# Kernel optimization log

Measured on AMD Instinct MI355X. Metric: run time of the kernel, lower is better.

The kernel has to match this reference:

```python
import jax, jax.numpy as jnp
import numpy as np


def conv2d(x, w, b, pad=0, groups=1):
    y = jax.lax.conv_general_dilated(
        x, w, (1, 1), [(pad, pad), (pad, pad)],
        dimension_numbers=('NCHW', 'OIHW', 'NCHW'), feature_group_count=groups)
    return y + b[None, :, None, None]


def layernorm(x, w, b, eps=1e-5):
    # per-pixel LayerNorm over channel dim (matches to_3d -> nn.LayerNorm(dim) -> to_4d)
    mu = x.mean(1, keepdims=True)
    var = ((x - mu) ** 2).mean(1, keepdims=True)
    return (x - mu) * jax.lax.rsqrt(var + eps) * w[None, :, None, None] + b[None, :, None, None]


def setup_inputs():
    key = jax.random.key(0)
    ks = jax.random.split(key, 16)
    B, C, H, W = 1, 64, 64, 64
    heads, dh = 8, 8
    inner = heads * dh          # 64
    hid_lc = 32                 # max(16, inner // 2)
    hid_f = 4 * C               # 256, ffn_expansion_factor = 4
    def s(k, shape, fan):
        return (jax.random.normal(k, shape, jnp.float32) / np.float32(np.sqrt(fan)))
    return {
        'x': jax.random.normal(ks[0], (B, C, H, W), jnp.float32),
        'luma': jax.random.uniform(ks[1], (B, 1, H, W), jnp.float32),
        'ln1_w': jnp.ones((C,), jnp.float32), 'ln1_b': jnp.zeros((C,), jnp.float32),
        'qkv_w': s(ks[2], (3 * inner, C, 1, 1), C), 'qkv_b': jnp.zeros((3 * inner,), jnp.float32),
        'proj_w': s(ks[3], (C, inner, 1, 1), inner), 'proj_b': jnp.zeros((C,), jnp.float32),
        'lc1_w': s(ks[4], (hid_lc, 1, 3, 3), 9), 'lc1_b': jnp.zeros((hid_lc,), jnp.float32),
        'lc2_w': s(ks[5], (hid_lc, hid_lc, 3, 3), 9 * hid_lc), 'lc2_b': jnp.zeros((hid_lc,), jnp.float32),
        'gam_w': s(ks[6], (inner, hid_lc, 1, 1), hid_lc), 'gam_b': jnp.zeros((inner,), jnp.float32),
        'bet_w': s(ks[7], (inner, hid_lc, 1, 1), hid_lc), 'bet_b': jnp.zeros((inner,), jnp.float32),
        'alpha': jnp.float32(0.1),
        'ln2_w': jnp.ones((C,), jnp.float32), 'ln2_b': jnp.zeros((C,), jnp.float32),
        'ffn1_w': s(ks[8], (hid_f, C, 1, 1), C), 'ffn1_b': jnp.zeros((hid_f,), jnp.float32),
        'dw_w': s(ks[9], (hid_f, 1, 3, 3), 9), 'dw_b': jnp.zeros((hid_f,), jnp.float32),
        'ffn2_w': s(ks[10], (C, hid_f, 1, 1), hid_f), 'ffn2_b': jnp.zeros((C,), jnp.float32),
    }


def reference(x, luma, ln1_w, ln1_b, qkv_w, qkv_b, proj_w, proj_b,
              lc1_w, lc1_b, lc2_w, lc2_b, gam_w, gam_b, bet_w, bet_b, alpha,
              ln2_w, ln2_b, ffn1_w, ffn1_b, dw_w, dw_b, ffn2_w, ffn2_b):
    B, C, H, W = x.shape
    heads = 8
    N = H * W
    # --- attention branch ---
    xn = layernorm(x, ln1_w, ln1_b)
    qkv = conv2d(xn, qkv_w, qkv_b)             # [B, 3*inner, H, W]
    inner = qkv.shape[1] // 3
    dh = inner // heads

    def to_bhnd(t):  # b (h d) x y -> b h (x y) d
        return t.reshape(B, heads, dh, N).transpose(0, 1, 3, 2)

    q, k, v = [to_bhnd(t) for t in jnp.split(qkv, 3, axis=1)]
    # luma conditioning
    h1 = jax.nn.relu(conv2d(luma, lc1_w, lc1_b, pad=1))
    h1 = jax.nn.relu(conv2d(h1, lc2_w, lc2_b, pad=1))
    g = to_bhnd(conv2d(h1, gam_w, gam_b))
    bt = to_bhnd(conv2d(h1, bet_w, bet_b))
    q = g * q + bt
    k = g * k + bt
    v = g * v + bt
    # additive luma bias on q (avg_pool2d 3x3, count_include_pad=True -> fixed /9)
    invL = 1.0 - luma
    invL = jax.lax.reduce_window(invL, 0.0, jax.lax.add, (1, 1, 3, 3), (1, 1, 1, 1),
                                 [(0, 0), (0, 0), (1, 1), (1, 1)]) / 9.0
    invL = invL.reshape(B, N)
    invL = invL - invL.mean(-1, keepdims=True)
    q = q + alpha * invL[:, None, :, None]
    scale = dh ** -0.5
    attn = jax.nn.softmax(jnp.einsum('bhid,bhjd->bhij', q, k) * scale, axis=-1)
    out = jnp.einsum('bhij,bhjd->bhid', attn, v)
    out = out.transpose(0, 1, 3, 2).reshape(B, inner, H, W)
    x = x + conv2d(out, proj_w, proj_b)
    # --- ConvFFN branch ---
    y = layernorm(x, ln2_w, ln2_b)
    y = conv2d(y, ffn1_w, ffn1_b)
    y = conv2d(y, dw_w, dw_b, pad=1, groups=y.shape[1])
    y = jax.nn.gelu(y, approximate=False)
    y = conv2d(y, ffn2_w, ffn2_b)
    return x + y
```

## Files before the change

### kernel.cpp

```cpp
#include <hip/hip_runtime.h>
#include <math.h>

#define NPIX 4096
#define IMG 64
#define NBLK 512

typedef __attribute__((ext_vector_type(8))) short bf16x8;
typedef __attribute__((ext_vector_type(4))) float floatx4;
typedef __attribute__((ext_vector_type(4))) unsigned int uintx4;

__device__ __forceinline__ unsigned int split_pack(float x) {
  unsigned int u = __float_as_uint(x);
  unsigned int hif = u & 0xffff0000u;
  float lof = x - __uint_as_float(hif);
  return (u >> 16) | (__float_as_uint(lof) & 0xffff0000u);
}

__device__ __forceinline__ unsigned int pack_hi2(float a, float b) {
  return __builtin_amdgcn_perm(__float_as_uint(b), __float_as_uint(a),
                               0x07060302u);
}

__device__ __forceinline__ void stA_f32(float* p, float v) {
  __hip_atomic_store(p, v, __ATOMIC_RELAXED, __HIP_MEMORY_SCOPE_AGENT);
}
__device__ __forceinline__ void stA_u32(void* p, unsigned int v) {
  __hip_atomic_store((unsigned int*)p, v, __ATOMIC_RELAXED,
                     __HIP_MEMORY_SCOPE_AGENT);
}
__device__ __forceinline__ void stA_u64(void* p, unsigned long long v) {
  __hip_atomic_store((unsigned long long*)p, v, __ATOMIC_RELAXED,
                     __HIP_MEMORY_SCOPE_AGENT);
}
__device__ __forceinline__ unsigned int ldA(const unsigned int* p) {
  return __hip_atomic_load(p, __ATOMIC_RELAXED, __HIP_MEMORY_SCOPE_AGENT);
}
__device__ __forceinline__ unsigned int addA(unsigned int* p) {
  return __hip_atomic_fetch_add(p, 1u, __ATOMIC_RELAXED,
                                __HIP_MEMORY_SCOPE_AGENT);
}

__device__ __forceinline__ void gbar(unsigned int* base, int bid) {
  __syncthreads();
  if (threadIdx.x == 0) {
    int g = bid >> 6;
    unsigned int* ga = base + g * 32;
    unsigned int old = addA(ga);
    if (old == 63u) {
      addA(base + 256);
      while (ldA(base + 256) < 8u) __builtin_amdgcn_s_sleep(1);
      stA_u32(ga + 16, 1u);
    } else {
      while (ldA(ga + 16) == 0u) __builtin_amdgcn_s_sleep(2);
    }
    asm volatile("" ::: "memory");
  }
  __syncthreads();
}

struct S1 {
  float lum[144];
  float sw1[288];
  float tin[32][100];
  float swt[4][32][9];
  float red[64];
};
struct S2 {
  float xs[64][32];
  float wsh[64][64];
  float h2s[32][32];
  float wgs[32][64];
  float wbs[32][64];
  float pss[8][32];
  float pqq[8][32];
  float mu[32];
  float rs[32];
};
struct S4 {
  float at[64][34];
  float wsh[64][64];
  float xsl[64][34];
  float ps[16][32];
  float pq[16][32];
  float mus[32];
  float rss[32];
};
struct S5 {
  float xs2[16][260];
  float wshT[32][260];
};
union SU {
  S1 s1;
  S2 s2;
  S4 s4;
  S5 s5;
};

__global__ void init_kernel(unsigned int* __restrict__ ctr,
                            unsigned short* __restrict__ cbuf) {
  int t = threadIdx.x;
#pragma unroll
  for (int i = 0; i < 8; i++) ctr[t + i * 256] = 0u;
  if (t < 16) cbuf[t] = (t < 8) ? 0x3F80 : 0;
}

__global__ __launch_bounds__(256, 3) void fused_kernel(
    const float* __restrict__ x, const float* __restrict__ luma,
    const float* __restrict__ lc1w, const float* __restrict__ lc1b,
    const float* __restrict__ lc2w, const float* __restrict__ lc2b,
    const float* __restrict__ ln1w, const float* __restrict__ ln1b,
    const float* __restrict__ qkvW, const float* __restrict__ qkvB,
    const float* __restrict__ gamW, const float* __restrict__ gamB,
    const float* __restrict__ betW, const float* __restrict__ betB,
    const float* __restrict__ alpha, const float* __restrict__ projW,
    const float* __restrict__ projB, const float* __restrict__ ln2w,
    const float* __restrict__ ln2b, const float* __restrict__ ffn1W,
    const float* __restrict__ ffn1B, const float* __restrict__ dww,
    const float* __restrict__ dwb, const float* __restrict__ ffn2W,
    const float* __restrict__ ffn2B, float* __restrict__ out,
    float* __restrict__ pooled, float* __restrict__ bsums,
    unsigned short* __restrict__ cbuf, unsigned short* __restrict__ qhl,
    unsigned short* __restrict__ khl, unsigned short* __restrict__ vthx,
    unsigned short* __restrict__ vtlx, float* __restrict__ pacc,
    float* __restrict__ pl, float* __restrict__ x1, float* __restrict__ f1,
    float* __restrict__ h2, unsigned int* __restrict__ ctr) {
  __shared__ SU u;
  int bid = blockIdx.x;
  int tid = threadIdx.x;

  {
    int tile = bid >> 3, ocg = bid & 7;
    int ty0 = (tile >> 3) * 8, tx0 = (tile & 7) * 8;
    float(&lum)[144] = u.s1.lum;
    float(&sw1)[288] = u.s1.sw1;
    float(&tin)[32][100] = u.s1.tin;
    float(&swt)[4][32][9] = u.s1.swt;
    float(&red)[64] = u.s1.red;
    if (tid < 144) {
      int py = tid / 12, px = tid - py * 12;
      int gy = ty0 + py - 2, gx = tx0 + px - 2;
      lum[tid] = (gy >= 0 && gy < IMG && gx >= 0 && gx < IMG)
                     ? luma[gy * IMG + gx]
                     : 0.f;
    }
    for (int idx = tid; idx < 288; idx += 256) sw1[idx] = lc1w[idx];
    for (int idx = tid; idx < 1152; idx += 256) {
      int o = idx / 288, r = idx - o * 288;
      swt[o][r / 9][r % 9] = lc2w[(ocg * 4 + o) * 288 + r];
    }
    __syncthreads();
    for (int idx = tid; idx < 3200; idx += 256) {
      int ic = idx / 100, pos = idx - ic * 100;
      int py = pos / 10, px = pos - py * 10;
      int gy = ty0 + py - 1, gx = tx0 + px - 1;
      float v = 0.f;
      if (gy >= 0 && gy < IMG && gx >= 0 && gx < IMG) {
        float s = lc1b[ic];
        const float* wp = &sw1[ic * 9];
#pragma unroll
        for (int dy = 0; dy < 3; dy++)
#pragma unroll
          for (int dx = 0; dx < 3; dx++)
            s = fmaf(wp[dy * 3 + dx], lum[(py + dy) * 12 + px + dx], s);
        v = fmaxf(s, 0.f);
      }
      tin[ic][pos] = v;
    }
    __syncthreads();
    int o = tid >> 6, pix = tid & 63;
    int ly = pix >> 3, lx = pix & 7;
    int p = (ty0 + ly) * IMG + tx0 + lx;
    float acc = lc2b[ocg * 4 + o];
    for (int ic = 0; ic < 32; ic++) {
      float v[9];
#pragma unroll
      for (int dy = 0; dy < 3; dy++)
#pragma unroll
        for (int dx = 0; dx < 3; dx++)
          v[dy * 3 + dx] = tin[ic][(ly + dy) * 10 + lx + dx];
#pragma unroll
      for (int t = 0; t < 9; t++) acc = fmaf(swt[o][ic][t], v[t], acc);
    }
    stA_f32(&h2[(ocg * 4 + o) * NPIX + p], fmaxf(acc, 0.f));
    if (ocg == 0) {
      if (tid < 64) {
        int gy = ty0 + ly, gx = tx0 + lx;
        float sv = 0.f;
#pragma unroll
        for (int dy = 0; dy < 3; dy++)
#pragma unroll
          for (int dx = 0; dx < 3; dx++)
            sv += lum[(ly + dy + 1) * 12 + lx + dx + 1];
        float cy = 3.f - (gy == 0 ? 1.f : 0.f) - (gy == 63 ? 1.f : 0.f);
        float cx = 3.f - (gx == 0 ? 1.f : 0.f) - (gx == 63 ? 1.f : 0.f);
        float pv = (cy * cx - sv) * (1.f / 9.f);
        stA_f32(&pooled[p], pv);
        red[tid] = pv;
      }
      __syncthreads();
      for (int st = 32; st > 0; st >>= 1) {
        if (tid < st) red[tid] += red[tid + st];
        __syncthreads();
      }
      if (tid == 0) stA_f32(&bsums[tile], red[0]);
    }
  }
  gbar(ctr + 0, bid);

  {
    const float QSCALE = 0.35355339059327376f * 1.4426950408889634f;
    float(&xs)[64][32] = u.s2.xs;
    float(&wsh)[64][64] = u.s2.wsh;
    float(&h2s)[32][32] = u.s2.h2s;
    float(&wgs)[32][64] = u.s2.wgs;
    float(&wbs)[32][64] = u.s2.wbs;
    float(&pss)[8][32] = u.s2.pss;
    float(&pqq)[8][32] = u.s2.pqq;
    float(&mu)[32] = u.s2.mu;
    float(&rs)[32] = u.s2.rs;
    int n0 = (bid & 127) * 32, part = bid >> 7;
    int m0 = (part < 2 ? part : 2) * 64;
    {
      int e = tid * 2;
      int c = e >> 3, off = (e & 7) * 4;
      *(float4*)&xs[c][off] = *(const float4*)&x[c * NPIX + n0 + off];
      int e1 = e + 1;
      int c1 = e1 >> 3, off1 = (e1 & 7) * 4;
      *(float4*)&xs[c1][off1] = *(const float4*)&x[c1 * NPIX + n0 + off1];
    }
    {
      int m = tid >> 2, kg = (tid & 3) * 16;
      const float4* wr = (const float4*)&qkvW[(m0 + m) * 64 + kg];
      float4 w0 = wr[0], w1 = wr[1], w2 = wr[2], w3 = wr[3];
      float wv[16] = {w0.x, w0.y, w0.z, w0.w, w1.x, w1.y, w1.z, w1.w,
                      w2.x, w2.y, w2.z, w2.w, w3.x, w3.y, w3.z, w3.w};
#pragma unroll
      for (int j = 0; j < 16; j++) wsh[kg + j][m] = wv[j];
    }
    {
      int k = tid >> 3, nf = (tid & 7) * 4;
      *(float4*)&h2s[k][nf] = *(const float4*)&h2[k * NPIX + n0 + nf];
    }
    {
      int m = tid >> 2, kg = (tid & 3) * 8;
      const float4* g0 = (const float4*)&gamW[m * 32 + kg];
      float4 a = g0[0], b4 = g0[1];
      float gv[8] = {a.x, a.y, a.z, a.w, b4.x, b4.y, b4.z, b4.w};
#pragma unroll
      for (int j = 0; j < 8; j++) wgs[kg + j][m] = gv[j];
      const float4* bb0 = (const float4*)&betW[m * 32 + kg];
      float4 c4 = bb0[0], d4 = bb0[1];
      float bv[8] = {c4.x, c4.y, c4.z, c4.w, d4.x, d4.y, d4.z, d4.w};
#pragma unroll
      for (int j = 0; j < 8; j++) wbs[kg + j][m] = bv[j];
    }
    __syncthreads();
    {
      int p = tid & 31, i = tid >> 5;
      float s = 0.f, q = 0.f;
#pragma unroll
      for (int j = 0; j < 8; j++) {
        float xv = xs[i * 8 + j][p];
        s += xv;
        q = fmaf(xv, xv, q);
      }
      pss[i][p] = s;
      pqq[i][p] = q;
    }
    __syncthreads();
    if (tid < 32) {
      float s = 0.f, q = 0.f;
#pragma unroll
      for (int i = 0; i < 8; i++) {
        s += pss[i][tid];
        q += pqq[i][tid];
      }
      float m = s * (1.f / 64.f);
      mu[tid] = m;
      rs[tid] = rsqrtf(q * (1.f / 64.f) - m * m + 1e-5f);
    }
    __syncthreads();
    {
      int c = tid >> 2, pg = (tid & 3) * 8;
      float wc = ln1w[c], bc = ln1b[c];
#pragma unroll
      for (int j = 0; j < 8; j++) {
        int p = pg + j;
        xs[c][p] = (xs[c][p] - mu[p]) * rs[p] * wc + bc;
      }
    }
    __syncthreads();
    int tx = tid & 15, ty = tid >> 4;
    float ga[4][2] = {}, ba[4][2] = {};
#pragma unroll 8
    for (int kk = 0; kk < 32; kk++) {
      float4 wg4 = *(const float4*)&wgs[kk][ty * 4];
      float4 wb4 = *(const float4*)&wbs[kk][ty * 4];
      float2 h22 = *(const float2*)&h2s[kk][tx * 2];
      float gv[4] = {wg4.x, wg4.y, wg4.z, wg4.w};
      float bv[4] = {wb4.x, wb4.y, wb4.z, wb4.w};
      float hv[2] = {h22.x, h22.y};
#pragma unroll
      for (int im = 0; im < 4; im++)
#pragma unroll
        for (int in = 0; in < 2; in++) {
          ga[im][in] = fmaf(gv[im], hv[in], ga[im][in]);
          ba[im][in] = fmaf(bv[im], hv[in], ba[im][in]);
        }
    }
#pragma unroll
    for (int im = 0; im < 4; im++) {
      int cc = ty * 4 + im;
      float gb = gamB[cc], bb2 = betB[cc];
#pragma unroll
      for (int in = 0; in < 2; in++) {
        ga[im][in] += gb;
        ba[im][in] += bb2;
      }
    }
    float acc[4][2] = {};
#pragma unroll 8
    for (int kk = 0; kk < 64; kk++) {
      float4 a = *(const float4*)&wsh[kk][ty * 4];
      float2 b2 = *(const float2*)&xs[kk][tx * 2];
      float av[4] = {a.x, a.y, a.z, a.w};
      float bv[2] = {b2.x, b2.y};
#pragma unroll
      for (int im = 0; im < 4; im++)
#pragma unroll
        for (int in = 0; in < 2; in++)
          acc[im][in] = fmaf(av[im], bv[in], acc[im][in]);
    }
    float val[4][2];
#pragma unroll
    for (int im = 0; im < 4; im++) {
      int cc = ty * 4 + im;
      float bv = qkvB[m0 + cc];
#pragma unroll
      for (int in = 0; in < 2; in++)
        val[im][in] = fmaf(ga[im][in], acc[im][in] + bv, ba[im][in]);
    }
    if (part == 0) {
      float msum = 0.f;
      for (int t = 0; t < 64; t++) msum += bsums[t];
      float mean = msum * (1.f / 4096.f);
      float a0 = alpha[0];
      const float2 pv = *(const float2*)&pooled[n0 + tx * 2];
      float iv[2] = {a0 * (pv.x - mean), a0 * (pv.y - mean)};
#pragma unroll
      for (int im = 0; im < 4; im++)
#pragma unroll
        for (int in = 0; in < 2; in++)
          val[im][in] = (val[im][in] + iv[in]) * QSCALE;
    }
    if (part < 2) {
      unsigned short* dst = (part == 0) ? qhl : khl;
      int hh = ty >> 1, d0 = (ty & 1) * 4;
#pragma unroll
      for (int in = 0; in < 2; in++) {
        int n = n0 + tx * 2 + in;
        unsigned int pk[4];
#pragma unroll
        for (int im = 0; im < 4; im++) pk[im] = split_pack(val[im][in]);
        short4 hi, lo;
        hi.x = (short)(pk[0] & 0xffffu); hi.y = (short)(pk[1] & 0xffffu);
        hi.z = (short)(pk[2] & 0xffffu); hi.w = (short)(pk[3] & 0xffffu);
        lo.x = (short)(pk[0] >> 16); lo.y = (short)(pk[1] >> 16);
        lo.z = (short)(pk[2] >> 16); lo.w = (short)(pk[3] >> 16);
        unsigned short* base = dst + ((size_t)(hh * NPIX + n) << 4) + d0;
        stA_u64(base, __builtin_bit_cast(unsigned long long, hi));
        stA_u64(base + 8, __builtin_bit_cast(unsigned long long, lo));
      }
    } else {
      int nq = n0 + tx * 2;
      int off0 = (nq >> 5) * 32 + ((nq >> 4) & 1) * 4 + ((nq >> 2) & 3) * 8 +
                 (nq & 3);
#pragma unroll
      for (int im = 0; im < 4; im++) {
        int cc = ty * 4 + im;
        unsigned int pk0 = split_pack(val[im][0]);
        unsigned int pk1 = split_pack(val[im][1]);
        if (part == 2) {
          short2 hi;
          hi.x = (short)(pk0 & 0xffffu);
          hi.y = (short)(pk1 & 0xffffu);
          stA_u32(vthx + (size_t)cc * NPIX + off0,
                  __builtin_bit_cast(unsigned int, hi));
        } else {
          short2 lo;
          lo.x = (short)(pk0 >> 16);
          lo.y = (short)(pk1 >> 16);
          stA_u32(vtlx + (size_t)cc * NPIX + off0,
                  __builtin_bit_cast(unsigned int, lo));
        }
      }
    }
  }
  gbar(ctr + 512, bid);

  {
    int wave = tid >> 6, lane = tid & 63;
    int g = lane >> 4, c = lane & 15;
    int h = (bid >> 4) & 7, jp = bid >> 7;
    int i0 = (bid & 15) * 256 + wave * 64;
    int jbase = jp * 1024;
    bf16x8 qB[4];
#pragma unroll
    for (int t = 0; t < 4; t++)
      qB[t] = *(const bf16x8*)(qhl +
                               ((size_t)(h * NPIX + i0 + t * 16 + c) << 4) +
                               ((g & 1) << 3));
    const unsigned short* kp =
        khl + ((size_t)(h * NPIX + jbase + c) << 4) + ((g >> 1) << 3);
    const unsigned short* vhp;
    const unsigned short* vlp;
    int vstep;
    if (c < 8) {
      vhp = vthx + (size_t)(h * 8 + c) * NPIX + jbase + (g << 3);
      vlp = vtlx + (size_t)(h * 8 + c) * NPIX + jbase + (g << 3);
      vstep = 32;
    } else {
      vhp = (c == 8) ? cbuf : (cbuf + 8);
      vlp = cbuf + 8;
      vstep = 0;
    }
    floatx4 zero4 = {0.f, 0.f, 0.f, 0.f};
    floatx4 aH[4], aM[4];
#pragma unroll
    for (int t = 0; t < 4; t++) {
      aH[t] = zero4;
      aM[t] = zero4;
    }
#pragma unroll 4
    for (int jt = 0; jt < 32; ++jt) {
      bf16x8 ka0 = *(const bf16x8*)kp;
      bf16x8 ka1 = *(const bf16x8*)(kp + 256);
      bf16x8 avh = *(const bf16x8*)vhp;
      bf16x8 avl = *(const bf16x8*)vlp;
      kp += 512;
      vhp += vstep;
      vlp += vstep;
#pragma unroll
      for (int t = 0; t < 4; t++) {
        floatx4 s0 = __builtin_amdgcn_mfma_f32_16x16x32_bf16(ka0, qB[t],
                                                             zero4, 0, 0, 0);
        floatx4 s1 = __builtin_amdgcn_mfma_f32_16x16x32_bf16(ka1, qB[t],
                                                             zero4, 0, 0, 0);
        float p0 = __builtin_amdgcn_exp2f(fminf(s0[0], 80.f));
        float p1 = __builtin_amdgcn_exp2f(fminf(s0[1], 80.f));
        float p2 = __builtin_amdgcn_exp2f(fminf(s0[2], 80.f));
        float p3 = __builtin_amdgcn_exp2f(fminf(s0[3], 80.f));
        float p4 = __builtin_amdgcn_exp2f(fminf(s1[0], 80.f));
        float p5 = __builtin_amdgcn_exp2f(fminf(s1[1], 80.f));
        float p6 = __builtin_amdgcn_exp2f(fminf(s1[2], 80.f));
        float p7 = __builtin_amdgcn_exp2f(fminf(s1[3], 80.f));
        uintx4 bh;
        bh.x = pack_hi2(p0, p1);
        bh.y = pack_hi2(p2, p3);
        bh.z = pack_hi2(p4, p5);
        bh.w = pack_hi2(p6, p7);
        bf16x8 pbh = __builtin_bit_cast(bf16x8, bh);
        aH[t] =
            __builtin_amdgcn_mfma_f32_16x16x32_bf16(avh, pbh, aH[t], 0, 0, 0);
        aM[t] =
            __builtin_amdgcn_mfma_f32_16x16x32_bf16(avl, pbh, aM[t], 0, 0, 0);
      }
    }
#pragma unroll
    for (int t = 0; t < 4; t++) {
      floatx4 o = aH[t] + aM[t];
      if (g < 2) {
        size_t b0 = (size_t)((jp * 8 + h) * NPIX + i0 + t * 16 + c);
        float2 lo2 = make_float2(o[0], o[1]);
        float2 hi2 = make_float2(o[2], o[3]);
        stA_u64(&pacc[b0 * 8 + g * 4],
                __builtin_bit_cast(unsigned long long, lo2));
        stA_u64(&pacc[b0 * 8 + g * 4 + 2],
                __builtin_bit_cast(unsigned long long, hi2));
      } else if (g == 2) {
        stA_f32(&pl[(size_t)((jp * 8 + h) * NPIX + i0 + t * 16 + c)], o[0]);
      }
    }
  }
  gbar(ctr + 1024, bid);

  {
    float(&at)[64][34] = u.s4.at;
    float(&wsh)[64][64] = u.s4.wsh;
    float(&xsl)[64][34] = u.s4.xsl;
    float(&ps)[16][32] = u.s4.ps;
    float(&pq)[16][32] = u.s4.pq;
    float(&mus)[32] = u.s4.mus;
    float(&rss)[32] = u.s4.rss;
    int n0 = (bid & 127) * 32;
    int ch = bid >> 7;
    int mm = tid >> 2, kg = (tid & 3) * 16;
    {
      const float4* wr = (const float4*)&projW[mm * 64 + kg];
      float4 w0 = wr[0], w1 = wr[1], w2 = wr[2], w3 = wr[3];
      float wv[16] = {w0.x, w0.y, w0.z, w0.w, w1.x, w1.y, w1.z, w1.w,
                      w2.x, w2.y, w2.z, w2.w, w3.x, w3.y, w3.z, w3.w};
#pragma unroll
      for (int j = 0; j < 16; j++) wsh[kg + j][mm] = wv[j];
    }
    {
      int hh = tid >> 5, nn = tid & 31;
      int i = n0 + nn;
      float L = 0.f, o[8] = {};
#pragma unroll
      for (int p = 0; p < 4; p++) {
        size_t base = (size_t)((p * 8 + hh) * NPIX + i);
        L += pl[base];
        const float4 a0 = *(const float4*)&pacc[base * 8];
        const float4 a1 = *(const float4*)&pacc[base * 8 + 4];
        o[0] += a0.x; o[1] += a0.y; o[2] += a0.z; o[3] += a0.w;
        o[4] += a1.x; o[5] += a1.y; o[6] += a1.z; o[7] += a1.w;
      }
      float inv = 1.f / L;
#pragma unroll
      for (int d = 0; d < 8; d++) at[hh * 8 + d][nn] = o[d] * inv;
    }
    __syncthreads();
    int mq = tid >> 4, pp = (tid & 15) * 2;
    float acc[4][2] = {};
#pragma unroll 8
    for (int k = 0; k < 64; k++) {
      float4 w4 = *(const float4*)&wsh[k][mq * 4];
      float2 b2 = *(const float2*)&at[k][pp];
      acc[0][0] = fmaf(w4.x, b2.x, acc[0][0]);
      acc[0][1] = fmaf(w4.x, b2.y, acc[0][1]);
      acc[1][0] = fmaf(w4.y, b2.x, acc[1][0]);
      acc[1][1] = fmaf(w4.y, b2.y, acc[1][1]);
      acc[2][0] = fmaf(w4.z, b2.x, acc[2][0]);
      acc[2][1] = fmaf(w4.z, b2.y, acc[2][1]);
      acc[3][0] = fmaf(w4.w, b2.x, acc[3][0]);
      acc[3][1] = fmaf(w4.w, b2.y, acc[3][1]);
    }
    float v[4][2], sn0 = 0.f, sn1 = 0.f, qn0 = 0.f, qn1 = 0.f;
#pragma unroll
    for (int im = 0; im < 4; im++) {
      int row = mq * 4 + im;
      float bpv = projB[row];
      const float2 xr = *(const float2*)&x[row * NPIX + n0 + pp];
      float v0 = acc[im][0] + bpv + xr.x;
      float v1 = acc[im][1] + bpv + xr.y;
      v[im][0] = v0;
      v[im][1] = v1;
      sn0 += v0;
      qn0 = fmaf(v0, v0, qn0);
      sn1 += v1;
      qn1 = fmaf(v1, v1, qn1);
    }
    if (ch == 0) {
#pragma unroll
      for (int im = 0; im < 4; im++)
        stA_u64(&x1[(mq * 4 + im) * NPIX + n0 + pp],
                __builtin_bit_cast(unsigned long long,
                                   make_float2(v[im][0], v[im][1])));
    }
    ps[mq][pp] = sn0;
    ps[mq][pp + 1] = sn1;
    pq[mq][pp] = qn0;
    pq[mq][pp + 1] = qn1;
    __syncthreads();
    {
      const float4* w1r = (const float4*)&ffn1W[(ch * 64 + mm) * 64 + kg];
      float4 u0 = w1r[0], u1 = w1r[1], u2 = w1r[2], u3 = w1r[3];
      float uv[16] = {u0.x, u0.y, u0.z, u0.w, u1.x, u1.y, u1.z, u1.w,
                      u2.x, u2.y, u2.z, u2.w, u3.x, u3.y, u3.z, u3.w};
#pragma unroll
      for (int j = 0; j < 16; j++) wsh[kg + j][mm] = uv[j];
    }
    if (tid < 32) {
      float s = 0.f, q = 0.f;
#pragma unroll
      for (int t = 0; t < 16; t++) {
        s += ps[t][tid];
        q += pq[t][tid];
      }
      float mu = s * (1.f / 64.f);
      mus[tid] = mu;
      rss[tid] = rsqrtf(q * (1.f / 64.f) - mu * mu + 1e-5f);
    }
    __syncthreads();
    {
      float mu0 = mus[pp], mu1v = mus[pp + 1];
      float rs0 = rss[pp], rs1v = rss[pp + 1];
#pragma unroll
      for (int im = 0; im < 4; im++) {
        int row = mq * 4 + im;
        float w2v = ln2w[row], b2v = ln2b[row];
        *(float2*)&xsl[row][pp] =
            make_float2((v[im][0] - mu0) * rs0 * w2v + b2v,
                        (v[im][1] - mu1v) * rs1v * w2v + b2v);
      }
    }
    __syncthreads();
    float a2[4][2] = {};
#pragma unroll 8
    for (int k = 0; k < 64; k++) {
      float4 w4 = *(const float4*)&wsh[k][mq * 4];
      float2 b2 = *(const float2*)&xsl[k][pp];
      a2[0][0] = fmaf(w4.x, b2.x, a2[0][0]);
      a2[0][1] = fmaf(w4.x, b2.y, a2[0][1]);
      a2[1][0] = fmaf(w4.y, b2.x, a2[1][0]);
      a2[1][1] = fmaf(w4.y, b2.y, a2[1][1]);
      a2[2][0] = fmaf(w4.z, b2.x, a2[2][0]);
      a2[2][1] = fmaf(w4.z, b2.y, a2[2][1]);
      a2[3][0] = fmaf(w4.w, b2.x, a2[3][0]);
      a2[3][1] = fmaf(w4.w, b2.y, a2[3][1]);
    }
#pragma unroll
    for (int im = 0; im < 4; im++) {
      int row = ch * 64 + mq * 4 + im;
      float bb = ffn1B[row];
      stA_u64(&f1[row * NPIX + n0 + pp],
              __builtin_bit_cast(unsigned long long,
                                 make_float2(a2[im][0] + bb, a2[im][1] + bb)));
    }
  }
  gbar(ctr + 1536, bid);

  {
    float(&xs2)[16][260] = u.s5.xs2;
    float(&wshT)[32][260] = u.s5.wshT;
    int n0 = (bid & 255) * 16, m0 = (bid >> 8) * 32;
    int y = n0 >> 6, x0 = n0 & 63;
    {
      int mm = tid >> 3, kg = (tid & 7) * 32;
      const float4* src = (const float4*)&ffn2W[(m0 + mm) * 256 + kg];
      float4* dst = (float4*)&wshT[mm][kg];
#pragma unroll
      for (int i = 0; i < 8; i++) dst[i] = src[i];
    }
    {
      int px4 = (tid & 3) * 4;
      int xabs = x0 + px4;
#pragma unroll
      for (int k = 0; k < 4; k++) {
        int c = (tid >> 2) + 64 * k;
        const float* base = f1 + c * NPIX;
        float wv[9];
#pragma unroll
        for (int i = 0; i < 9; i++) wv[i] = dww[c * 9 + i];
        float bc = dwb[c];
        float a[4] = {bc, bc, bc, bc};
#pragma unroll
        for (int dy = 0; dy < 3; dy++) {
          int yy = y + dy - 1;
          if (yy < 0 || yy > 63) continue;
          const float* row = base + yy * IMG + xabs;
          float4 mid = *(const float4*)row;
          float left = (xabs > 0) ? row[-1] : 0.f;
          float right = (xabs + 4 < IMG) ? row[4] : 0.f;
          float win[6] = {left, mid.x, mid.y, mid.z, mid.w, right};
#pragma unroll
          for (int o = 0; o < 4; o++)
#pragma unroll
            for (int dx = 0; dx < 3; dx++)
              a[o] = fmaf(wv[dy * 3 + dx], win[o + dx], a[o]);
        }
#pragma unroll
        for (int o = 0; o < 4; o++)
          xs2[px4 + o][c] =
              0.5f * a[o] * (1.f + erff(a[o] * 0.70710678118654752f));
      }
    }
    __syncthreads();
    int m = tid >> 3, np = (tid & 7) * 2;
    float a0 = 0.f, a1 = 0.f;
#pragma unroll 4
    for (int k4 = 0; k4 < 64; k4++) {
      float4 w4 = *(const float4*)&wshT[m][k4 * 4];
      float4 xa = *(const float4*)&xs2[np][k4 * 4];
      float4 xb = *(const float4*)&xs2[np + 1][k4 * 4];
      a0 = fmaf(w4.x, xa.x, a0);
      a1 = fmaf(w4.x, xb.x, a1);
      a0 = fmaf(w4.y, xa.y, a0);
      a1 = fmaf(w4.y, xb.y, a1);
      a0 = fmaf(w4.z, xa.z, a0);
      a1 = fmaf(w4.z, xb.z, a1);
      a0 = fmaf(w4.w, xa.w, a0);
      a1 = fmaf(w4.w, xb.w, a1);
    }
    int row = m0 + m;
    float bv = ffn2B[row];
    const float2 rr = *(const float2*)&x1[row * NPIX + n0 + np];
    *(float2*)&out[row * NPIX + n0 + np] =
        make_float2(a0 + bv + rr.x, a1 + bv + rr.y);
  }
}

extern "C" void kernel_launch(void* const* d_in, const int* in_sizes, int n_in,
                              void* d_out, int out_size, void* d_ws,
                              size_t ws_size, hipStream_t stream) {
  const float* x      = (const float*)d_in[0];
  const float* luma   = (const float*)d_in[1];
  const float* ln1_w  = (const float*)d_in[2];
  const float* ln1_b  = (const float*)d_in[3];
  const float* qkv_w  = (const float*)d_in[4];
  const float* qkv_b  = (const float*)d_in[5];
  const float* proj_w = (const float*)d_in[6];
  const float* proj_b = (const float*)d_in[7];
  const float* lc1_w  = (const float*)d_in[8];
  const float* lc1_b  = (const float*)d_in[9];
  const float* lc2_w  = (const float*)d_in[10];
  const float* lc2_b  = (const float*)d_in[11];
  const float* gam_w  = (const float*)d_in[12];
  const float* gam_b  = (const float*)d_in[13];
  const float* bet_w  = (const float*)d_in[14];
  const float* bet_b  = (const float*)d_in[15];
  const float* alpha  = (const float*)d_in[16];
  const float* ln2_w  = (const float*)d_in[17];
  const float* ln2_b  = (const float*)d_in[18];
  const float* ffn1_w = (const float*)d_in[19];
  const float* ffn1_b = (const float*)d_in[20];
  const float* dw_w   = (const float*)d_in[21];
  const float* dw_b   = (const float*)d_in[22];
  const float* ffn2_w = (const float*)d_in[23];
  const float* ffn2_b = (const float*)d_in[24];
  float* out = (float*)d_out;

  float* w = (float*)d_ws;
  float* pooled = w + 0;
  float* bsums  = w + 4096;
  unsigned short* cbuf = (unsigned short*)(w + 4160);
  unsigned short* qhl  = (unsigned short*)(w + 12416);
  unsigned short* khl  = (unsigned short*)(w + 274560);
  unsigned short* vthx = (unsigned short*)(w + 536704);
  unsigned short* vtlx = (unsigned short*)(w + 667776);
  float* pacc = w + 798848;
  float* pl   = w + 2896000;
  float* x1   = w + 3158144;
  float* f1   = w + 3420288;
  float* h2   = w + 4468864;
  unsigned int* ctr = (unsigned int*)(w + 4599936);

  init_kernel<<<1, 256, 0, stream>>>(ctr, cbuf);
  fused_kernel<<<dim3(NBLK), 256, 0, stream>>>(
      x, luma, lc1_w, lc1_b, lc2_w, lc2_b, ln1_w, ln1_b, qkv_w, qkv_b, gam_w,
      gam_b, bet_w, bet_b, alpha, proj_w, proj_b, ln2_w, ln2_b, ffn1_w, ffn1_b,
      dw_w, dw_b, ffn2_w, ffn2_b, out, pooled, bsums, cbuf, qhl, khl,
      vthx, vtlx, pacc, pl, x1, f1, h2, ctr);
}
```

Baseline: 202.0 us.

## Double persistent grid to 1024 blocks and halve per-block work in every stage

```diff
diff --git a/kernel.cpp b/kernel.cpp
--- a/kernel.cpp
+++ b/kernel.cpp
@@ -3,7 +3,7 @@
 
 #define NPIX 4096
 #define IMG 64
-#define NBLK 512
+#define NBLK 1024
 
 typedef __attribute__((ext_vector_type(8))) short bf16x8;
 typedef __attribute__((ext_vector_type(4))) float floatx4;
@@ -45,10 +45,9 @@
   if (threadIdx.x == 0) {
     int g = bid >> 6;
     unsigned int* ga = base + g * 32;
-    unsigned int old = addA(ga);
-    if (old == 63u) {
-      addA(base + 256);
-      while (ldA(base + 256) < 8u) __builtin_amdgcn_s_sleep(1);
+    if (addA(ga) == 63u) {
+      addA(base + 512);
+      while (ldA(base + 512) < 16u) __builtin_amdgcn_s_sleep(1);
       stA_u32(ga + 16, 1u);
     } else {
       while (ldA(ga + 16) == 0u) __builtin_amdgcn_s_sleep(2);
@@ -59,35 +58,35 @@
 }
 
 struct S1 {
-  float lum[144];
+  float lum[96];
   float sw1[288];
-  float tin[32][100];
+  float tin[32][60];
   float swt[4][32][9];
-  float red[64];
+  float red[32];
 };
 struct S2 {
   float xs[64][32];
-  float wsh[64][64];
+  float wsh[64][32];
   float h2s[32][32];
-  float wgs[32][64];
-  float wbs[32][64];
-  float pss[8][32];
-  float pqq[8][32];
+  float wgs[32][32];
+  float wbs[32][32];
+  float pss[8][33];
+  float pqq[8][33];
   float mu[32];
   float rs[32];
 };
 struct S4 {
-  float at[64][34];
+  float at[64][17];
   float wsh[64][64];
-  float xsl[64][34];
-  float ps[16][32];
-  float pq[16][32];
-  float mus[32];
-  float rss[32];
+  float xsl[64][17];
+  float ps[16][17];
+  float pq[16][17];
+  float mus[16];
+  float rss[16];
 };
 struct S5 {
   float xs2[16][260];
-  float wshT[32][260];
+  float wshT[16][260];
 };
 union SU {
   S1 s1;
@@ -100,11 +99,11 @@
                             unsigned short* __restrict__ cbuf) {
   int t = threadIdx.x;
 #pragma unroll
-  for (int i = 0; i < 8; i++) ctr[t + i * 256] = 0u;
+  for (int i = 0; i < 16; i++) ctr[t + i * 256] = 0u;
   if (t < 16) cbuf[t] = (t < 8) ? 0x3F80 : 0;
 }
 
-__global__ __launch_bounds__(256, 3) void fused_kernel(
+__global__ __launch_bounds__(256, 4) void fused_kernel(
     const float* __restrict__ x, const float* __restrict__ luma,
     const float* __restrict__ lc1w, const float* __restrict__ lc1b,
     const float* __restrict__ lc2w, const float* __restrict__ lc2b,
@@ -130,13 +129,13 @@
 
   {
     int tile = bid >> 3, ocg = bid & 7;
-    int ty0 = (tile >> 3) * 8, tx0 = (tile & 7) * 8;
-    float(&lum)[144] = u.s1.lum;
+    int ty0 = (tile >> 3) * 4, tx0 = (tile & 7) * 8;
+    float(&lum)[96] = u.s1.lum;
     float(&sw1)[288] = u.s1.sw1;
-    float(&tin)[32][100] = u.s1.tin;
+    float(&tin)[32][60] = u.s1.tin;
     float(&swt)[4][32][9] = u.s1.swt;
-    float(&red)[64] = u.s1.red;
-    if (tid < 144) {
+    float(&red)[32] = u.s1.red;
+    if (tid < 96) {
       int py = tid / 12, px = tid - py * 12;
       int gy = ty0 + py - 2, gx = tx0 + px - 2;
       lum[tid] = (gy >= 0 && gy < IMG && gx >= 0 && gx < IMG)
@@ -149,8 +148,8 @@
       swt[o][r / 9][r % 9] = lc2w[(ocg * 4 + o) * 288 + r];
     }
     __syncthreads();
-    for (int idx = tid; idx < 3200; idx += 256) {
-      int ic = idx / 100, pos = idx - ic * 100;
+    for (int idx = tid; idx < 1920; idx += 256) {
+      int ic = idx / 60, pos = idx - ic * 60;
       int py = pos / 10, px = pos - py * 10;
       int gy = ty0 + py - 1, gx = tx0 + px - 1;
       float v = 0.f;
@@ -167,23 +166,27 @@
       tin[ic][pos] = v;
     }
     __syncthreads();
-    int o = tid >> 6, pix = tid & 63;
-    int ly = pix >> 3, lx = pix & 7;
-    int p = (ty0 + ly) * IMG + tx0 + lx;
-    float acc = lc2b[ocg * 4 + o];
-    for (int ic = 0; ic < 32; ic++) {
-      float v[9];
-#pragma unroll
-      for (int dy = 0; dy < 3; dy++)
-#pragma unroll
-        for (int dx = 0; dx < 3; dx++)
-          v[dy * 3 + dx] = tin[ic][(ly + dy) * 10 + lx + dx];
-#pragma unroll
-      for (int t = 0; t < 9; t++) acc = fmaf(swt[o][ic][t], v[t], acc);
-    }
-    stA_f32(&h2[(ocg * 4 + o) * NPIX + p], fmaxf(acc, 0.f));
+    if (tid < 128) {
+      int o = tid >> 5, pix = tid & 31;
+      int ly = pix >> 3, lx = pix & 7;
+      int p = (ty0 + ly) * IMG + tx0 + lx;
+      float acc = lc2b[ocg * 4 + o];
+      for (int ic = 0; ic < 32; ic++) {
+        float v[9];
+#pragma unroll
+        for (int dy = 0; dy < 3; dy++)
+#pragma unroll
+          for (int dx = 0; dx < 3; dx++)
+            v[dy * 3 + dx] = tin[ic][(ly + dy) * 10 + lx + dx];
+#pragma unroll
+        for (int t = 0; t < 9; t++) acc = fmaf(swt[o][ic][t], v[t], acc);
+      }
+      stA_f32(&h2[(ocg * 4 + o) * NPIX + p], fmaxf(acc, 0.f));
+    }
     if (ocg == 0) {
-      if (tid < 64) {
+      if (tid < 32) {
+        int ly = tid >> 3, lx = tid & 7;
+        int p = (ty0 + ly) * IMG + tx0 + lx;
         int gy = ty0 + ly, gx = tx0 + lx;
         float sv = 0.f;
 #pragma unroll
@@ -198,7 +201,7 @@
         red[tid] = pv;
       }
       __syncthreads();
-      for (int st = 32; st > 0; st >>= 1) {
+      for (int st = 16; st > 0; st >>= 1) {
         if (tid < st) red[tid] += red[tid + st];
         __syncthreads();
       }
@@ -210,16 +213,17 @@
   {
     const float QSCALE = 0.35355339059327376f * 1.4426950408889634f;
     float(&xs)[64][32] = u.s2.xs;
-    float(&wsh)[64][64] = u.s2.wsh;
+    float(&wsh)[64][32] = u.s2.wsh;
     float(&h2s)[32][32] = u.s2.h2s;
-    float(&wgs)[32][64] = u.s2.wgs;
-    float(&wbs)[32][64] = u.s2.wbs;
-    float(&pss)[8][32] = u.s2.pss;
-    float(&pqq)[8][32] = u.s2.pqq;
+    float(&wgs)[32][32] = u.s2.wgs;
+    float(&wbs)[32][32] = u.s2.wbs;
+    float(&pss)[8][33] = u.s2.pss;
+    float(&pqq)[8][33] = u.s2.pqq;
     float(&mu)[32] = u.s2.mu;
     float(&rs)[32] = u.s2.rs;
     int n0 = (bid & 127) * 32, part = bid >> 7;
-    int m0 = (part < 2 ? part : 2) * 64;
+    int kind = part >> 1, mh = part & 1;
+    int m0 = (kind < 2 ? kind * 64 : 128) + mh * 32;
     {
       int e = tid * 2;
       int c = e >> 3, off = (e & 7) * 4;
@@ -229,30 +233,25 @@
       *(float4*)&xs[c1][off1] = *(const float4*)&x[c1 * NPIX + n0 + off1];
     }
     {
-      int m = tid >> 2, kg = (tid & 3) * 16;
+      int m = tid >> 3, kg = (tid & 7) * 8;
       const float4* wr = (const float4*)&qkvW[(m0 + m) * 64 + kg];
-      float4 w0 = wr[0], w1 = wr[1], w2 = wr[2], w3 = wr[3];
-      float wv[16] = {w0.x, w0.y, w0.z, w0.w, w1.x, w1.y, w1.z, w1.w,
-                      w2.x, w2.y, w2.z, w2.w, w3.x, w3.y, w3.z, w3.w};
-#pragma unroll
-      for (int j = 0; j < 16; j++) wsh[kg + j][m] = wv[j];
+      float4 w0 = wr[0], w1 = wr[1];
+      float wv[8] = {w0.x, w0.y, w0.z, w0.w, w1.x, w1.y, w1.z, w1.w};
+#pragma unroll
+      for (int j = 0; j < 8; j++) wsh[kg + j][m] = wv[j];
     }
     {
       int k = tid >> 3, nf = (tid & 7) * 4;
       *(float4*)&h2s[k][nf] = *(const float4*)&h2[k * NPIX + n0 + nf];
     }
     {
-      int m = tid >> 2, kg = (tid & 3) * 8;
-      const float4* g0 = (const float4*)&gamW[m * 32 + kg];
-      float4 a = g0[0], b4 = g0[1];
-      float gv[8] = {a.x, a.y, a.z, a.w, b4.x, b4.y, b4.z, b4.w};
-#pragma unroll
-      for (int j = 0; j < 8; j++) wgs[kg + j][m] = gv[j];
-      const float4* bb0 = (const float4*)&betW[m * 32 + kg];
-      float4 c4 = bb0[0], d4 = bb0[1];
-      float bv[8] = {c4.x, c4.y, c4.z, c4.w, d4.x, d4.y, d4.z, d4.w};
-#pragma unroll
-      for (int j = 0; j < 8; j++) wbs[kg + j][m] = bv[j];
+      int m = tid >> 3, kg = (tid & 7) * 4;
+      float4 a = *(const float4*)&gamW[(mh * 32 + m) * 32 + kg];
+      wgs[kg + 0][m] = a.x; wgs[kg + 1][m] = a.y;
+      wgs[kg + 2][m] = a.z; wgs[kg + 3][m] = a.w;
+      float4 b4 = *(const float4*)&betW[(mh * 32 + m) * 32 + kg];
+      wbs[kg + 0][m] = b4.x; wbs[kg + 1][m] = b4.y;
+      wbs[kg + 2][m] = b4.z; wbs[kg + 3][m] = b4.w;
     }
     __syncthreads();
     {
@@ -291,17 +290,17 @@
     }
     __syncthreads();
     int tx = tid & 15, ty = tid >> 4;
-    float ga[4][2] = {}, ba[4][2] = {};
+    float ga[2][2] = {}, ba[2][2] = {};
 #pragma unroll 8
     for (int kk = 0; kk < 32; kk++) {
-      float4 wg4 = *(const float4*)&wgs[kk][ty * 4];
-      float4 wb4 = *(const float4*)&wbs[kk][ty * 4];
+      float2 wg2 = *(const float2*)&wgs[kk][ty * 2];
+      float2 wb2 = *(const float2*)&wbs[kk][ty * 2];
       float2 h22 = *(const float2*)&h2s[kk][tx * 2];
-      float gv[4] = {wg4.x, wg4.y, wg4.z, wg4.w};
-      float bv[4] = {wb4.x, wb4.y, wb4.z, wb4.w};
+      float gv[2] = {wg2.x, wg2.y};
+      float bv[2] = {wb2.x, wb2.y};
       float hv[2] = {h22.x, h22.y};
 #pragma unroll
-      for (int im = 0; im < 4; im++)
+      for (int im = 0; im < 2; im++)
 #pragma unroll
         for (int in = 0; in < 2; in++) {
           ga[im][in] = fmaf(gv[im], hv[in], ga[im][in]);
@@ -309,8 +308,8 @@
         }
     }
 #pragma unroll
-    for (int im = 0; im < 4; im++) {
-      int cc = ty * 4 + im;
+    for (int im = 0; im < 2; im++) {
+      int cc = mh * 32 + ty * 2 + im;
       float gb = gamB[cc], bb2 = betB[cc];
 #pragma unroll
       for (int in = 0; in < 2; in++) {
@@ -318,95 +317,87 @@
         ba[im][in] += bb2;
       }
     }
-    float acc[4][2] = {};
+    float acc[2][2] = {};
 #pragma unroll 8
     for (int kk = 0; kk < 64; kk++) {
-      float4 a = *(const float4*)&wsh[kk][ty * 4];
+      float2 a2r = *(const float2*)&wsh[kk][ty * 2];
       float2 b2 = *(const float2*)&xs[kk][tx * 2];
-      float av[4] = {a.x, a.y, a.z, a.w};
+      float av[2] = {a2r.x, a2r.y};
       float bv[2] = {b2.x, b2.y};
 #pragma unroll
-      for (int im = 0; im < 4; im++)
+      for (int im = 0; im < 2; im++)
 #pragma unroll
         for (int in = 0; in < 2; in++)
           acc[im][in] = fmaf(av[im], bv[in], acc[im][in]);
     }
-    float val[4][2];
-#pragma unroll
-    for (int im = 0; im < 4; im++) {
-      int cc = ty * 4 + im;
-      float bv = qkvB[m0 + cc];
+    float val[2][2];
+#pragma unroll
+    for (int im = 0; im < 2; im++) {
+      int cc = mh * 32 + ty * 2 + im;
+      float bv = qkvB[(kind < 2 ? kind : 2) * 64 + cc];
 #pragma unroll
       for (int in = 0; in < 2; in++)
         val[im][in] = fmaf(ga[im][in], acc[im][in] + bv, ba[im][in]);
     }
-    if (part == 0) {
+    if (kind == 0) {
       float msum = 0.f;
-      for (int t = 0; t < 64; t++) msum += bsums[t];
+      for (int t = 0; t < 128; t++) msum += bsums[t];
       float mean = msum * (1.f / 4096.f);
       float a0 = alpha[0];
       const float2 pv = *(const float2*)&pooled[n0 + tx * 2];
       float iv[2] = {a0 * (pv.x - mean), a0 * (pv.y - mean)};
 #pragma unroll
-      for (int im = 0; im < 4; im++)
+      for (int im = 0; im < 2; im++)
 #pragma unroll
         for (int in = 0; in < 2; in++)
           val[im][in] = (val[im][in] + iv[in]) * QSCALE;
     }
-    if (part < 2) {
-      unsigned short* dst = (part == 0) ? qhl : khl;
-      int hh = ty >> 1, d0 = (ty & 1) * 4;
+    if (kind < 2) {
+      unsigned short* dst = (kind == 0) ? qhl : khl;
+      int mloc = mh * 32 + ty * 2;
+      int hh = mloc >> 3, d0 = mloc & 7;
 #pragma unroll
       for (int in = 0; in < 2; in++) {
         int n = n0 + tx * 2 + in;
-        unsigned int pk[4];
-#pragma unroll
-        for (int im = 0; im < 4; im++) pk[im] = split_pack(val[im][in]);
-        short4 hi, lo;
-        hi.x = (short)(pk[0] & 0xffffu); hi.y = (short)(pk[1] & 0xffffu);
-        hi.z = (short)(pk[2] & 0xffffu); hi.w = (short)(pk[3] & 0xffffu);
-        lo.x = (short)(pk[0] >> 16); lo.y = (short)(pk[1] >> 16);
-        lo.z = (short)(pk[2] >> 16); lo.w = (short)(pk[3] >> 16);
+        unsigned int pk0 = split_pack(val[0][in]);
+        unsigned int pk1 = split_pack(val[1][in]);
+        unsigned int hi2 = (pk0 & 0xffffu) | (pk1 << 16);
+        unsigned int lo2 = (pk0 >> 16) | (pk1 & 0xffff0000u);
         unsigned short* base = dst + ((size_t)(hh * NPIX + n) << 4) + d0;
-        stA_u64(base, __builtin_bit_cast(unsigned long long, hi));
-        stA_u64(base + 8, __builtin_bit_cast(unsigned long long, lo));
+        stA_u32(base, hi2);
+        stA_u32(base + 8, lo2);
       }
     } else {
       int nq = n0 + tx * 2;
       int off0 = (nq >> 5) * 32 + ((nq >> 4) & 1) * 4 + ((nq >> 2) & 3) * 8 +
                  (nq & 3);
 #pragma unroll
-      for (int im = 0; im < 4; im++) {
-        int cc = ty * 4 + im;
+      for (int im = 0; im < 2; im++) {
+        int cc = mh * 32 + ty * 2 + im;
         unsigned int pk0 = split_pack(val[im][0]);
         unsigned int pk1 = split_pack(val[im][1]);
-        if (part == 2) {
-          short2 hi;
-          hi.x = (short)(pk0 & 0xffffu);
-          hi.y = (short)(pk1 & 0xffffu);
-          stA_u32(vthx + (size_t)cc * NPIX + off0,
-                  __builtin_bit_cast(unsigned int, hi));
+        if (kind == 2) {
+          unsigned int hi2 = (pk0 & 0xffffu) | (pk1 << 16);
+          stA_u32(vthx + (size_t)cc * NPIX + off0, hi2);
         } else {
-          short2 lo;
-          lo.x = (short)(pk0 >> 16);
-          lo.y = (short)(pk1 >> 16);
-          stA_u32(vtlx + (size_t)cc * NPIX + off0,
-                  __builtin_bit_cast(unsigned int, lo));
+          unsigned int lo2 = (pk0 >> 16) | (pk1 & 0xffff0000u);
+          stA_u32(vtlx + (size_t)cc * NPIX + off0, lo2);
         }
       }
     }
   }
-  gbar(ctr + 512, bid);
+  gbar(ctr + 1024, bid);
 
   {
     int wave = tid >> 6, lane = tid & 63;
     int g = lane >> 4, c = lane & 15;
-    int h = (bid >> 4) & 7, jp = bid >> 7;
-    int i0 = (bid & 15) * 256 + wave * 64;
+    int u3 = bid & 31, itile = bid >> 5;
+    int h = u3 >> 2, jp = u3 & 3;
+    int i0 = itile * 128 + wave * 32;
     int jbase = jp * 1024;
-    bf16x8 qB[4];
-#pragma unroll
-    for (int t = 0; t < 4; t++)
+    bf16x8 qB[2];
+#pragma unroll
+    for (int t = 0; t < 2; t++)
       qB[t] = *(const bf16x8*)(qhl +
                                ((size_t)(h * NPIX + i0 + t * 16 + c) << 4) +
                                ((g & 1) << 3));
@@ -425,9 +416,9 @@
       vstep = 0;
     }
     floatx4 zero4 = {0.f, 0.f, 0.f, 0.f};
-    floatx4 aH[4], aM[4];
-#pragma unroll
-    for (int t = 0; t < 4; t++) {
+    floatx4 aH[2], aM[2];
+#pragma unroll
+    for (int t = 0; t < 2; t++) {
       aH[t] = zero4;
       aM[t] = zero4;
     }
@@ -441,7 +432,7 @@
       vhp += vstep;
       vlp += vstep;
 #pragma unroll
-      for (int t = 0; t < 4; t++) {
+      for (int t = 0; t < 2; t++) {
         floatx4 s0 = __builtin_amdgcn_mfma_f32_16x16x32_bf16(ka0, qB[t],
                                                              zero4, 0, 0, 0);
         floatx4 s1 = __builtin_amdgcn_mfma_f32_16x16x32_bf16(ka1, qB[t],
@@ -467,7 +458,7 @@
       }
     }
 #pragma unroll
-    for (int t = 0; t < 4; t++) {
+    for (int t = 0; t < 2; t++) {
       floatx4 o = aH[t] + aM[t];
       if (g < 2) {
         size_t b0 = (size_t)((jp * 8 + h) * NPIX + i0 + t * 16 + c);
@@ -482,18 +473,18 @@
       }
     }
   }
-  gbar(ctr + 1024, bid);
+  gbar(ctr + 2048, bid);
 
   {
-    float(&at)[64][34] = u.s4.at;
+    float(&at)[64][17] = u.s4.at;
     float(&wsh)[64][64] = u.s4.wsh;
-    float(&xsl)[64][34] = u.s4.xsl;
-    float(&ps)[16][32] = u.s4.ps;
-    float(&pq)[16][32] = u.s4.pq;
-    float(&mus)[32] = u.s4.mus;
-    float(&rss)[32] = u.s4.rss;
-    int n0 = (bid & 127) * 32;
-    int ch = bid >> 7;
+    float(&xsl)[64][17] = u.s4.xsl;
+    float(&ps)[16][17] = u.s4.ps;
+    float(&pq)[16][17] = u.s4.pq;
+    float(&mus)[16] = u.s4.mus;
+    float(&rss)[16] = u.s4.rss;
+    int n0 = (bid & 255) * 16;
+    int ch = bid >> 8;
     int mm = tid >> 2, kg = (tid & 3) * 16;
     {
       const float4* wr = (const float4*)&projW[mm * 64 + kg];
@@ -504,64 +495,48 @@
       for (int j = 0; j < 16; j++) wsh[kg + j][mm] = wv[j];
     }
     {
-      int hh = tid >> 5, nn = tid & 31;
+      int hh8 = (tid >> 4) & 7, dgrp = tid >> 7, nn = tid & 15;
       int i = n0 + nn;
-      float L = 0.f, o[8] = {};
+      float L = 0.f, o[4] = {};
 #pragma unroll
       for (int p = 0; p < 4; p++) {
-        size_t base = (size_t)((p * 8 + hh) * NPIX + i);
+        size_t base = (size_t)((p * 8 + hh8) * NPIX + i);
         L += pl[base];
-        const float4 a0 = *(const float4*)&pacc[base * 8];
-        const float4 a1 = *(const float4*)&pacc[base * 8 + 4];
+        const float4 a0 = *(const float4*)&pacc[base * 8 + dgrp * 4];
         o[0] += a0.x; o[1] += a0.y; o[2] += a0.z; o[3] += a0.w;
-        o[4] += a1.x; o[5] += a1.y; o[6] += a1.z; o[7] += a1.w;
       }
       float inv = 1.f / L;
 #pragma unroll
-      for (int d = 0; d < 8; d++) at[hh * 8 + d][nn] = o[d] * inv;
-    }
-    __syncthreads();
-    int mq = tid >> 4, pp = (tid & 15) * 2;
-    float acc[4][2] = {};
+      for (int d = 0; d < 4; d++) at[hh8 * 8 + dgrp * 4 + d][nn] = o[d] * inv;
+    }
+    __syncthreads();
+    int ty = tid >> 4, tx = tid & 15;
+    float acc[4] = {};
 #pragma unroll 8
     for (int k = 0; k < 64; k++) {
-      float4 w4 = *(const float4*)&wsh[k][mq * 4];
-      float2 b2 = *(const float2*)&at[k][pp];
-      acc[0][0] = fmaf(w4.x, b2.x, acc[0][0]);
-      acc[0][1] = fmaf(w4.x, b2.y, acc[0][1]);
-      acc[1][0] = fmaf(w4.y, b2.x, acc[1][0]);
-      acc[1][1] = fmaf(w4.y, b2.y, acc[1][1]);
-      acc[2][0] = fmaf(w4.z, b2.x, acc[2][0]);
-      acc[2][1] = fmaf(w4.z, b2.y, acc[2][1]);
-      acc[3][0] = fmaf(w4.w, b2.x, acc[3][0]);
-      acc[3][1] = fmaf(w4.w, b2.y, acc[3][1]);
-    }
-    float v[4][2], sn0 = 0.f, sn1 = 0.f, qn0 = 0.f, qn1 = 0.f;
+      float4 w4 = *(const float4*)&wsh[k][ty * 4];
+      float b = at[k][tx];
+      acc[0] = fmaf(w4.x, b, acc[0]);
+      acc[1] = fmaf(w4.y, b, acc[1]);
+      acc[2] = fmaf(w4.z, b, acc[2]);
+      acc[3] = fmaf(w4.w, b, acc[3]);
+    }
+    float v[4], sn = 0.f, qn = 0.f;
 #pragma unroll
     for (int im = 0; im < 4; im++) {
-      int row = mq * 4 + im;
-      float bpv = projB[row];
-      const float2 xr = *(const float2*)&x[row * NPIX + n0 + pp];
-      float v0 = acc[im][0] + bpv + xr.x;
-      float v1 = acc[im][1] + bpv + xr.y;
-      v[im][0] = v0;
-      v[im][1] = v1;
-      sn0 += v0;
-      qn0 = fmaf(v0, v0, qn0);
-      sn1 += v1;
-      qn1 = fmaf(v1, v1, qn1);
+      int row = ty * 4 + im;
+      float vv = acc[im] + projB[row] + x[row * NPIX + n0 + tx];
+      v[im] = vv;
+      sn += vv;
+      qn = fmaf(vv, vv, qn);
     }
     if (ch == 0) {
 #pragma unroll
       for (int im = 0; im < 4; im++)
-        stA_u64(&x1[(mq * 4 + im) * NPIX + n0 + pp],
-                __builtin_bit_cast(unsigned long long,
-                                   make_float2(v[im][0], v[im][1])));
-    }
-    ps[mq][pp] = sn0;
-    ps[mq][pp + 1] = sn1;
-    pq[mq][pp] = qn0;
-    pq[mq][pp + 1] = qn1;
+        stA_f32(&x1[(ty * 4 + im) * NPIX + n0 + tx], v[im]);
+    }
+    ps[ty][tx] = sn;
+    pq[ty][tx] = qn;
     __syncthreads();
     {
       const float4* w1r = (const float4*)&ffn1W[(ch * 64 + mm) * 64 + kg];
@@ -571,7 +546,7 @@
 #pragma unroll
       for (int j = 0; j < 16; j++) wsh[kg + j][mm] = uv[j];
     }
-    if (tid < 32) {
+    if (tid < 16) {
       float s = 0.f, q = 0.f;
 #pragma unroll
       for (int t = 0; t < 16; t++) {
@@ -584,54 +559,43 @@
     }
     __syncthreads();
     {
-      float mu0 = mus[pp], mu1v = mus[pp + 1];
-      float rs0 = rss[pp], rs1v = rss[pp + 1];
+      float mu0 = mus[tx], rs0 = rss[tx];
 #pragma unroll
       for (int im = 0; im < 4; im++) {
-        int row = mq * 4 + im;
-        float w2v = ln2w[row], b2v = ln2b[row];
-        *(float2*)&xsl[row][pp] =
-            make_float2((v[im][0] - mu0) * rs0 * w2v + b2v,
-                        (v[im][1] - mu1v) * rs1v * w2v + b2v);
-      }
-    }
-    __syncthreads();
-    float a2[4][2] = {};
+        int row = ty * 4 + im;
+        xsl[row][tx] = (v[im] - mu0) * rs0 * ln2w[row] + ln2b[row];
+      }
+    }
+    __syncthreads();
+    float a2[4] = {};
 #pragma unroll 8
     for (int k = 0; k < 64; k++) {
-      float4 w4 = *(const float4*)&wsh[k][mq * 4];
-      float2 b2 = *(const float2*)&xsl[k][pp];
-      a2[0][0] = fmaf(w4.x, b2.x, a2[0][0]);
-      a2[0][1] = fmaf(w4.x, b2.y, a2[0][1]);
-      a2[1][0] = fmaf(w4.y, b2.x, a2[1][0]);
-      a2[1][1] = fmaf(w4.y, b2.y, a2[1][1]);
-      a2[2][0] = fmaf(w4.z, b2.x, a2[2][0]);
-      a2[2][1] = fmaf(w4.z, b2.y, a2[2][1]);
-      a2[3][0] = fmaf(w4.w, b2.x, a2[3][0]);
-      a2[3][1] = fmaf(w4.w, b2.y, a2[3][1]);
+      float4 w4 = *(const float4*)&wsh[k][ty * 4];
+      float b = xsl[k][tx];
+      a2[0] = fmaf(w4.x, b, a2[0]);
+      a2[1] = fmaf(w4.y, b, a2[1]);
+      a2[2] = fmaf(w4.z, b, a2[2]);
+      a2[3] = fmaf(w4.w, b, a2[3]);
     }
 #pragma unroll
     for (int im = 0; im < 4; im++) {
-      int row = ch * 64 + mq * 4 + im;
-      float bb = ffn1B[row];
-      stA_u64(&f1[row * NPIX + n0 + pp],
-              __builtin_bit_cast(unsigned long long,
-                                 make_float2(a2[im][0] + bb, a2[im][1] + bb)));
+      int row = ch * 64 + ty * 4 + im;
+      stA_f32(&f1[row * NPIX + n0 + tx], a2[im] + ffn1B[row]);
     }
   }
-  gbar(ctr + 1536, bid);
+  gbar(ctr + 3072, bid);
 
   {
     float(&xs2)[16][260] = u.s5.xs2;
-    float(&wshT)[32][260] = u.s5.wshT;
-    int n0 = (bid & 255) * 16, m0 = (bid >> 8) * 32;
+    float(&wshT)[16][260] = u.s5.wshT;
+    int n0 = (bid & 255) * 16, m0 = (bid >> 8) * 16;
     int y = n0 >> 6, x0 = n0 & 63;
     {
-      int mm = tid >> 3, kg = (tid & 7) * 32;
+      int mm = tid >> 4, kg = (tid & 15) * 16;
       const float4* src = (const float4*)&ffn2W[(m0 + mm) * 256 + kg];
       float4* dst = (float4*)&wshT[mm][kg];
 #pragma unroll
-      for (int i = 0; i < 8; i++) dst[i] = src[i];
+      for (int i = 0; i < 4; i++) dst[i] = src[i];
     }
     {
       int px4 = (tid & 3) * 4;
@@ -667,27 +631,19 @@
       }
     }
     __syncthreads();
-    int m = tid >> 3, np = (tid & 7) * 2;
-    float a0 = 0.f, a1 = 0.f;
+    int m = tid >> 4, np = tid & 15;
+    float a0 = 0.f;
 #pragma unroll 4
     for (int k4 = 0; k4 < 64; k4++) {
       float4 w4 = *(const float4*)&wshT[m][k4 * 4];
       float4 xa = *(const float4*)&xs2[np][k4 * 4];
-      float4 xb = *(const float4*)&xs2[np + 1][k4 * 4];
       a0 = fmaf(w4.x, xa.x, a0);
-      a1 = fmaf(w4.x, xb.x, a1);
       a0 = fmaf(w4.y, xa.y, a0);
-      a1 = fmaf(w4.y, xb.y, a1);
       a0 = fmaf(w4.z, xa.z, a0);
-      a1 = fmaf(w4.z, xb.z, a1);
       a0 = fmaf(w4.w, xa.w, a0);
-      a1 = fmaf(w4.w, xb.w, a1);
     }
     int row = m0 + m;
-    float bv = ffn2B[row];
-    const float2 rr = *(const float2*)&x1[row * NPIX + n0 + np];
-    *(float2*)&out[row * NPIX + n0 + np] =
-        make_float2(a0 + bv + rr.x, a1 + bv + rr.y);
+    out[row * NPIX + n0 + np] = a0 + ffn2B[row] + x1[row * NPIX + n0 + np];
   }
 }
 
@@ -724,7 +680,7 @@
   float* w = (float*)d_ws;
   float* pooled = w + 0;
   float* bsums  = w + 4096;
-  unsigned short* cbuf = (unsigned short*)(w + 4160);
+  unsigned short* cbuf = (unsigned short*)(w + 4224);
   unsigned short* qhl  = (unsigned short*)(w + 12416);
   unsigned short* khl  = (unsigned short*)(w + 274560);
   unsigned short* vthx = (unsigned short*)(w + 536704);
```

Measured after the change: 222.5 us. +10.2%, slower.
